# Optimization experiments

Hardware: AMD Instinct MI355X
Metric: run time of the kernel (lower is better)

The kernel has to match this reference:

```python
import jax, jax.numpy as jnp
from jax import lax
import numpy as np

N_ATOMS, N_BONDS, N_GRAPHS = 8192, 32768, 256
EMBED, HIDDEN, DEPTH = 32, 256, 10
ATOM_VOCAB, BOND_VOCAB = 200, 10


def setup_inputs() -> dict:
    key = jax.random.key(0)
    ks = jax.random.split(key, 16)
    f = lambda k, *sh: jax.random.normal(k, sh, dtype=jnp.float32) * 0.05
    return {
        "atom_features": jax.random.randint(ks[0], (N_ATOMS,), 0, ATOM_VOCAB),
        "bond_features": jax.random.randint(ks[1], (N_BONDS,), 0, BOND_VOCAB),
        "adjacency_matrix": jax.random.randint(ks[2], (N_ATOMS, N_ATOMS), 0, 2, dtype=jnp.int32),
        "batch_indices": jax.random.randint(ks[3], (N_ATOMS,), 0, N_GRAPHS),
        "atom_emb": f(ks[4], ATOM_VOCAB, EMBED),
        "bond_emb": f(ks[5], BOND_VOCAB, EMBED),
        "msg_W": f(ks[6], DEPTH, HIDDEN, 2 * EMBED),
        "msg_b": f(ks[7], DEPTH, HIDDEN),
        "gru_Wih": f(ks[8], DEPTH, 3 * EMBED, HIDDEN),
        "gru_Whh": f(ks[9], DEPTH, 3 * EMBED, EMBED),
        "gru_bih": f(ks[10], DEPTH, 3 * EMBED),
        "gru_bhh": f(ks[11], DEPTH, 3 * EMBED),
        "pool_W": f(ks[12], HIDDEN, EMBED),
        "pool_b": f(ks[13], HIDDEN),
    }


def _gmpn(atom_emb, bond_emb, msg_W, msg_b, gru_Wih, gru_Whh, gru_bih, gru_bhh,
          pool_W, pool_b, atom_features, bond_features, adjacency_matrix, batch_indices):
    H = atom_emb[atom_features]                       # [N, E]
    A = (adjacency_matrix > 0).astype(H.dtype)        # [N, N] 0/1
    deg = A.sum(axis=1)                               # [N]
    has_nb = deg > 0
    inv_deg = jnp.where(has_nb, 1.0 / jnp.maximum(deg, 1.0), 0.0)[:, None]

    def layer(h, params):
        W, b, wih, whh, b_ih, b_hh = params
        # mean_j Linear([h_i ; h_j]) = W1 h_i + W2 mean_j h_j + b
        neigh_mean = (A @ h) * inv_deg                # [N, E]
        W1, W2 = W[:, :EMBED], W[:, EMBED:]
        msg = h @ W1.T + neigh_mean @ W2.T + b        # [N, HIDDEN]
        msg = jnp.where(has_nb[:, None], msg, 0.0)    # zero message if no neighbors
        # single-step GRU: input=msg, hidden state=h
        gi = msg @ wih.T + b_ih
        gh = h @ whh.T + b_hh
        ir, iz, inn = jnp.split(gi, 3, axis=-1)
        hr, hz, hn = jnp.split(gh, 3, axis=-1)
        r = jax.nn.sigmoid(ir + hr)
        z = jax.nn.sigmoid(iz + hz)
        n = jnp.tanh(inn + r * hn)
        h_new = (1.0 - z) * n + z * h                 # [N, E]
        return h_new, None

    H, _ = lax.scan(layer, H, (msg_W, msg_b, gru_Wih, gru_Whh, gru_bih, gru_bhh))

    # per-graph mean pooling (zeros for empty graphs), then global_pool linear
    seg_sum = jax.ops.segment_sum(H, batch_indices, num_segments=N_GRAPHS)
    cnt = jax.ops.segment_sum(jnp.ones((H.shape[0],), H.dtype), batch_indices, num_segments=N_GRAPHS)
    graph_mean = jnp.where(cnt[:, None] > 0, seg_sum / jnp.maximum(cnt, 1.0)[:, None], 0.0)
    graph_embeddings = graph_mean @ pool_W.T + pool_b  # [G, HIDDEN]

    bond_embeddings = bond_emb[bond_features]          # [B, E]
    return H, bond_embeddings, graph_embeddings


def reference(atom_features, bond_features, adjacency_matrix, batch_indices,
              atom_emb, bond_emb, msg_W, msg_b, gru_Wih, gru_Whh, gru_bih, gru_bhh,
              pool_W, pool_b):
    return _gmpn(atom_emb, bond_emb, msg_W, msg_b, gru_Wih, gru_Whh, gru_bih, gru_bhh,
                 pool_W, pool_b, atom_features, bond_features, adjacency_matrix, batch_indices)
```

## Files before the change

kernel.cpp:

```cpp
#include <hip/hip_runtime.h>
#include <stdint.h>

typedef __bf16 bf16x8 __attribute__((ext_vector_type(8)));
typedef float f32x4 __attribute__((ext_vector_type(4)));

__device__ __forceinline__ float b2f(unsigned short u){
  unsigned int t = ((unsigned int)u) << 16;
  return __builtin_bit_cast(float, t);
}
__device__ __forceinline__ unsigned short f2b(float f){
  unsigned int x = __builtin_bit_cast(unsigned int, f);
  x = x + 0x7FFFu + ((x >> 16) & 1u);
  return (unsigned short)(x >> 16);
}
__device__ __forceinline__ void spread8(unsigned int B, unsigned int w[4]){
  unsigned int m = __umul24(B, 0x8001u);
  w[0] = __umul24(m & 0x00010001u, 0x3F80u);
  w[1] = __umul24(m & 0x00040004u, 0x0FE0u);
  w[2] = __umul24(m & 0x00100010u, 0x03F8u);
  w[3] = __umul24(m & 0x00400040u, 0x00FEu);
}
__device__ __forceinline__ float fsig(float x){ return 1.f/(1.f + __expf(-x)); }
__device__ __forceinline__ float ftanh(float x){ return 1.f - 2.f/(__expf(2.f*x) + 1.f); }

__global__ void k_prep(const void* s_msgW, const void* s_msgb, const void* s_wih,
                       const void* s_whh, const void* s_bih, const void* s_bhh,
                       const void* s_poolW, const void* s_poolb,
                       const unsigned short* __restrict__ aemb_u16,
                       unsigned short* __restrict__ cw,
                       int* __restrict__ deg, float* __restrict__ seg,
                       float* __restrict__ cnt, int* __restrict__ flag){
  int b = blockIdx.x, t = threadIdx.x;
  unsigned int uu = aemb_u16[2*t];
  int e = (int)((uu >> 7) & 0xFF);
  unsigned long long vote = __ballot(e >= 100 && e <= 127);
  int isb = (__popcll(vote) > 32) ? 1 : 0;
  if (b < 1771){
    int id = b*256 + t;
    if (id < 453248){
      const void* src; int off;
      if      (id < 163840){ src = s_msgW;  off = id; }
      else if (id < 166400){ src = s_msgb;  off = id - 163840; }
      else if (id < 412160){ src = s_wih;   off = id - 166400; }
      else if (id < 442880){ src = s_whh;   off = id - 412160; }
      else if (id < 443840){ src = s_bih;   off = id - 442880; }
      else if (id < 444800){ src = s_bhh;   off = id - 443840; }
      else if (id < 452992){ src = s_poolW; off = id - 444800; }
      else                 { src = s_poolb; off = id - 452992; }
      cw[id] = isb ? ((const unsigned short*)src)[off]
                   : f2b(((const float*)src)[off]);
    }
  } else {
    int id2 = (b - 1771)*256 + t;
    if (id2 < 8192){ deg[id2] = 0; seg[id2] = 0.f; }
    if (id2 < 256) cnt[id2] = 0.f;
    if (b == 1771 && t == 0) flag[0] = isb;
  }
}

__global__ void k_pack(const int* __restrict__ adj, unsigned int* __restrict__ mask3,
                       int* __restrict__ deg){
  int tid = blockIdx.x*256 + threadIdx.x;
  int rb  = tid >> 12;
  int rem = tid & 4095;
  int kgg = rem >> 6;
  int L   = rem & 63;
  int lc = L & 15, q = L >> 4;
  int row = rb*16 + lc;
  const int* arow = adj + (size_t)row*8192 + kgg*128 + q*8;
  unsigned int dw = 0; int pc = 0;
  #pragma unroll
  for (int s=0;s<4;s++){
    const int* p = arow + s*32;
    unsigned int b = 0;
    #pragma unroll
    for (int t=0;t<8;t++) b |= (p[t] > 0 ? 1u : 0u) << t;
    dw |= b << (8*s);
    pc += __popc(b);
  }
  mask3[tid] = dw;
  pc += __shfl_xor(pc, 16);
  pc += __shfl_xor(pc, 32);
  if (q == 0) atomicAdd(deg + row, pc);
}

__global__ void k_bond(const int* __restrict__ bft, const void* __restrict__ braw,
                       const int* __restrict__ flag,
                       unsigned short* __restrict__ outB16, float* __restrict__ outB32){
  int id = blockIdx.x*256 + threadIdx.x;
  int e = id >> 5, c = id & 31;
  int idx = bft[e]*32 + c;
  if (flag[0]) outB16[id] = ((const unsigned short*)braw)[idx];
  else         outB32[id] = ((const float*)braw)[idx];
}

__global__ void k_embed(const int* __restrict__ af, const void* __restrict__ araw,
                        const int* __restrict__ flag,
                        float* __restrict__ hf32, uint4* __restrict__ hfrag){
  __shared__ __align__(16) float sh[512];
  int t = threadIdx.x;
  int r = t >> 5, c = t & 31;
  int row = blockIdx.x*16 + r;
  int idx = af[row]*32 + c;
  float f;
  if (flag[0]) f = b2f(((const unsigned short*)araw)[idx]);
  else         f = ((const float*)araw)[idx];
  hf32[row*32 + c] = f;
  sh[r*32 + c] = f;
  __syncthreads();
  if (t < 64){
    int nt = t >> 5, Lq = t & 31;
    int ks32 = blockIdx.x >> 1, half = blockIdx.x & 1;
    int col = nt*16 + (Lq & 15);
    int rbase = (Lq >> 4)*8;
    unsigned int w[4];
    #pragma unroll
    for (int p=0;p<4;p++){
      unsigned int lo = f2b(sh[(rbase + 2*p    )*32 + col]);
      unsigned int hi = f2b(sh[(rbase + 2*p + 1)*32 + col]);
      w[p] = lo | (hi << 16);
    }
    hfrag[(ks32*2 + nt)*64 + half*32 + Lq] = make_uint4(w[0],w[1],w[2],w[3]);
  }
}

__launch_bounds__(512)
__global__ void k_layer(const unsigned int* __restrict__ mask3,
                        const uint4* __restrict__ hfragIn,
                        unsigned int* __restrict__ hfragOut,
                        float* __restrict__ hf32,
                        const int* __restrict__ deg,
                        const unsigned short* __restrict__ msgW,
                        const unsigned short* __restrict__ msgb,
                        const unsigned short* __restrict__ wih,
                        const unsigned short* __restrict__ whh,
                        const unsigned short* __restrict__ bih,
                        const unsigned short* __restrict__ bhh,
                        const int* __restrict__ bidx,
                        float* __restrict__ seg, float* __restrict__ cnt,
                        unsigned short* __restrict__ out16, float* __restrict__ out32,
                        const int* __restrict__ flag, int last)
{
  __shared__ __align__(16) char uni[33792];
  __shared__ __align__(16) unsigned short sA[32][72];
  __shared__ __align__(16) unsigned short smsg[32][264];
  __shared__ int sdeg[32];

  const int t = threadIdx.x;
  const int b = blockIdx.x;
  const int w = t >> 6, L = t & 63;
  const int q = L >> 4, lc = L & 15;
  const int rowbase = b*32;

  const int r0 = t >> 4;
  const int cl = t & 15;
  const int r  = rowbase + r0;
  const int isb = flag[0];
  const int dgr = deg[r];
  const float invr = dgr > 0 ? 1.f/(float)dgr : 0.f;
  float h0 = hf32[r*32 + cl];
  float h1 = hf32[r*32 + 16 + cl];
  sA[r0][cl]    = f2b(h0);
  sA[r0][16+cl] = f2b(h1);
  if (cl == 0) sdeg[r0] = dgr;

  {
    f32x4 a00={0,0,0,0}, a01={0,0,0,0}, a10={0,0,0,0}, a11={0,0,0,0};
    const unsigned int* mp = mask3 + (size_t)b*8192 + w*512 + L;
    const uint4* bp = hfragIn + (size_t)w*4096 + L;
    for (int g=0; g<8; g++){
      unsigned int mw0 = mp[g*64];
      unsigned int mw1 = mp[4096 + g*64];
      #pragma unroll
      for (int s=0; s<4; s++){
        int ks = g*4 + s;
        uint4 u0 = bp[ks*128];
        uint4 u1 = bp[ks*128 + 64];
        union { unsigned int u[4]; bf16x8 v; } A0, A1, B0, B1;
        spread8((mw0 >> (8*s)) & 0xFFu, A0.u);
        spread8((mw1 >> (8*s)) & 0xFFu, A1.u);
        B0.u[0]=u0.x; B0.u[1]=u0.y; B0.u[2]=u0.z; B0.u[3]=u0.w;
        B1.u[0]=u1.x; B1.u[1]=u1.y; B1.u[2]=u1.z; B1.u[3]=u1.w;
        a00 = __builtin_amdgcn_mfma_f32_16x16x32_bf16(A0.v, B0.v, a00, 0,0,0);
        a01 = __builtin_amdgcn_mfma_f32_16x16x32_bf16(A0.v, B1.v, a01, 0,0,0);
        a10 = __builtin_amdgcn_mfma_f32_16x16x32_bf16(A1.v, B0.v, a10, 0,0,0);
        a11 = __builtin_amdgcn_mfma_f32_16x16x32_bf16(A1.v, B1.v, a11, 0,0,0);
      }
    }
    float* sp = (float*)uni + w*1056;
    #pragma unroll
    for (int rg=0; rg<4; rg++){
      int rw = q*4 + rg;
      sp[rw*33 + lc]         = a00[rg];
      sp[rw*33 + 16 + lc]    = a01[rg];
      sp[(16+rw)*33 + lc]    = a10[rg];
      sp[(16+rw)*33 + 16+lc] = a11[rg];
    }
  }
  __syncthreads();
  {
    const float* spf = (const float*)uni;
    float s0 = 0.f, s1 = 0.f;
    #pragma unroll
    for (int ww=0; ww<8; ww++){
      s0 += spf[ww*1056 + r0*33 + cl];
      s1 += spf[ww*1056 + r0*33 + 16 + cl];
    }
    sA[r0][32+cl] = f2b(s0*invr);
    sA[r0][48+cl] = f2b(s1*invr);
  }
  __syncthreads();
  {
    int rt = w & 1, ntb = (w >> 1)*4;
    union { uint4 u; bf16x8 v; } A0, A1;
    A0.u = *(const uint4*)&sA[rt*16 + lc][q*8];
    A1.u = *(const uint4*)&sA[rt*16 + lc][32 + q*8];
    #pragma unroll
    for (int i=0; i<4; i++){
      int nt = ntb + i;
      union { uint4 u; bf16x8 v; } B0, B1;
      B0.u = *(const uint4*)(msgW + (size_t)(nt*16 + lc)*64 + q*8);
      B1.u = *(const uint4*)(msgW + (size_t)(nt*16 + lc)*64 + 32 + q*8);
      f32x4 am = {0,0,0,0};
      am = __builtin_amdgcn_mfma_f32_16x16x32_bf16(A0.v, B0.v, am, 0,0,0);
      am = __builtin_amdgcn_mfma_f32_16x16x32_bf16(A1.v, B1.v, am, 0,0,0);
      float bv = b2f(msgb[nt*16 + lc]);
      #pragma unroll
      for (int rg=0; rg<4; rg++){
        int rw = rt*16 + q*4 + rg;
        float v = am[rg] + bv;
        if (sdeg[rw] == 0) v = 0.f;
        smsg[rw][nt*16 + lc] = f2b(v);
      }
    }
  }
  __syncthreads();
  {
    float* sgi = (float*)uni;
    float* sgh = (float*)(uni + 12800);
    if (w < 6){
      int nt = w;
      f32x4 g0 = {0,0,0,0}, g1 = {0,0,0,0};
      #pragma unroll
      for (int ks=0; ks<8; ks++){
        union { uint4 u; bf16x8 v; } A0, A1, B;
        B.u  = *(const uint4*)(wih + (size_t)(nt*16 + lc)*256 + ks*32 + q*8);
        A0.u = *(const uint4*)&smsg[lc][ks*32 + q*8];
        A1.u = *(const uint4*)&smsg[16 + lc][ks*32 + q*8];
        g0 = __builtin_amdgcn_mfma_f32_16x16x32_bf16(A0.v, B.v, g0, 0,0,0);
        g1 = __builtin_amdgcn_mfma_f32_16x16x32_bf16(A1.v, B.v, g1, 0,0,0);
      }
      #pragma unroll
      for (int rg=0; rg<4; rg++){
        sgi[(q*4+rg)*100      + nt*16 + lc] = g0[rg];
        sgi[(16+q*4+rg)*100   + nt*16 + lc] = g1[rg];
      }
    } else {
      int rt = w - 6;
      union { uint4 u; bf16x8 v; } A;
      A.u = *(const uint4*)&sA[rt*16 + lc][q*8];
      #pragma unroll
      for (int nt=0; nt<6; nt++){
        union { uint4 u; bf16x8 v; } B;
        B.u = *(const uint4*)(whh + (size_t)(nt*16 + lc)*32 + q*8);
        f32x4 hh = {0,0,0,0};
        hh = __builtin_amdgcn_mfma_f32_16x16x32_bf16(A.v, B.v, hh, 0,0,0);
        #pragma unroll
        for (int rg=0; rg<4; rg++)
          sgh[(rt*16 + q*4+rg)*100 + nt*16 + lc] = hh[rg];
      }
    }
  }
  __syncthreads();
  {
    const float* sgi = (const float*)uni;
    const float* sgh = (const float*)(uni + 12800);
    float ir0 = sgi[r0*100 + cl]    + b2f(bih[cl]),    hr0 = sgh[r0*100 + cl]    + b2f(bhh[cl]);
    float iz0 = sgi[r0*100 + 32+cl] + b2f(bih[32+cl]), hz0 = sgh[r0*100 + 32+cl] + b2f(bhh[32+cl]);
    float in0 = sgi[r0*100 + 64+cl] + b2f(bih[64+cl]), hn0 = sgh[r0*100 + 64+cl] + b2f(bhh[64+cl]);
    float ir1 = sgi[r0*100 + 16+cl] + b2f(bih[16+cl]), hr1 = sgh[r0*100 + 16+cl] + b2f(bhh[16+cl]);
    float iz1 = sgi[r0*100 + 48+cl] + b2f(bih[48+cl]), hz1 = sgh[r0*100 + 48+cl] + b2f(bhh[48+cl]);
    float in1 = sgi[r0*100 + 80+cl] + b2f(bih[80+cl]), hn1 = sgh[r0*100 + 80+cl] + b2f(bhh[80+cl]);
    float rr0 = fsig(ir0 + hr0), zz0 = fsig(iz0 + hz0);
    float rr1 = fsig(ir1 + hr1), zz1 = fsig(iz1 + hz1);
    float nn0 = ftanh(in0 + rr0*hn0);
    float nn1 = ftanh(in1 + rr1*hn1);
    h0 = (1.f - zz0)*nn0 + zz0*h0;
    h1 = (1.f - zz1)*nn1 + zz1*h1;
    hf32[r*32 + cl]      = h0;
    hf32[r*32 + 16 + cl] = h1;
    unsigned int m0 = f2b(h0), m1 = f2b(h1);
    unsigned int p0 = (unsigned int)__shfl_xor((int)m0, 16);
    unsigned int p1 = (unsigned int)__shfl_xor((int)m1, 16);
    if ((r & 1) == 0){
      int ks32 = r >> 5;
      int Lf = ((r >> 3) & 3)*16 + cl;
      int pidx = (r & 7) >> 1;
      hfragOut[((ks32*2 + 0)*64 + Lf)*4 + pidx] = m0 | (p0 << 16);
      hfragOut[((ks32*2 + 1)*64 + Lf)*4 + pidx] = m1 | (p1 << 16);
    }
    if (last){
      if (isb){ out16[r*32 + cl] = (unsigned short)m0; out16[r*32 + 16 + cl] = (unsigned short)m1; }
      else    { out32[r*32 + cl] = h0; out32[r*32 + 16 + cl] = h1; }
      int gb = bidx[r];
      atomicAdd(seg + gb*32 + cl, h0);
      atomicAdd(seg + gb*32 + 16 + cl, h1);
      if (cl == 0) atomicAdd(cnt + gb, 1.f);
    }
  }
}

__global__ void k_pool(const float* __restrict__ seg, const float* __restrict__ cnt,
                       const unsigned short* __restrict__ pw, const unsigned short* __restrict__ pb,
                       const int* __restrict__ flag,
                       unsigned short* __restrict__ outG16, float* __restrict__ outG32){
  int g = blockIdx.x, o = threadIdx.x;
  float cv = cnt[g];
  float ic = cv > 0.f ? 1.f/cv : 0.f;
  float s = 0.f;
  #pragma unroll
  for (int c=0;c<32;c++) s += seg[g*32+c]*ic*b2f(pw[o*32+c]);
  s += b2f(pb[o]);
  if (flag[0]) outG16[g*256 + o] = f2b(s);
  else         outG32[g*256 + o] = s;
}

extern "C" void kernel_launch(void* const* d_in, const int* in_sizes, int n_in,
                              void* d_out, int out_size, void* d_ws, size_t ws_size,
                              hipStream_t stream){
  const int* af   = (const int*)d_in[0];
  const int* bft  = (const int*)d_in[1];
  const int* adj  = (const int*)d_in[2];
  const int* bidx = (const int*)d_in[3];

  char* ws = (char*)d_ws;
  unsigned int*   mask3  = (unsigned int*)(ws + 0);
  unsigned int*   hfrag0 = (unsigned int*)(ws + 8388608);
  unsigned int*   hfrag1 = (unsigned int*)(ws + 8912896);
  float*          hf32   = (float*)(ws + 9437184);
  int*            deg    = (int*)(ws + 10485760);
  float*          seg    = (float*)(ws + 10518528);
  float*          cnt    = (float*)(ws + 10551296);
  int*            flag   = (int*)(ws + 10552320);
  unsigned short* cw     = (unsigned short*)(ws + 10552384);

  unsigned short* o16 = (unsigned short*)d_out;
  float*          o32 = (float*)d_out;

  k_prep<<<1803, 256, 0, stream>>>(d_in[6], d_in[7], d_in[8], d_in[9], d_in[10],
                                   d_in[11], d_in[12], d_in[13],
                                   (const unsigned short*)d_in[4],
                                   cw, deg, seg, cnt, flag);
  k_pack<<<8192, 256, 0, stream>>>(adj, mask3, deg);
  k_bond<<<4096, 256, 0, stream>>>(bft, d_in[5], flag, o16 + 262144, o32 + 262144);
  k_embed<<<512, 512, 0, stream>>>(af, d_in[4], flag, hf32, (uint4*)hfrag0);

  for (int d = 0; d < 10; d++){
    const uint4*  hin  = (const uint4*)((d & 1) ? hfrag1 : hfrag0);
    unsigned int* hout = (d & 1) ? hfrag0 : hfrag1;
    k_layer<<<256, 512, 0, stream>>>(mask3, hin, hout, hf32, deg,
                                     cw + (size_t)d*16384,        cw + 163840 + d*256,
                                     cw + 166400 + (size_t)d*24576, cw + 412160 + d*3072,
                                     cw + 442880 + d*96,          cw + 443840 + d*96,
                                     bidx, seg, cnt, o16, o32, flag, (d == 9) ? 1 : 0);
  }
  k_pool<<<256, 256, 0, stream>>>(seg, cnt, cw + 444800, cw + 452992, flag,
                                  o16 + 1310720, o32 + 1310720);
}
```

Baseline: 535.3 us.

## Halve rows per layer block to double grid, vectorize adjacency packing loads

The layer kernel now handles 16 atom rows per block instead of 32 and launches 512 blocks, so more CUs are busy on a 256-CU-class GPU. Each block's shared memory roughly halves and a min-blocks launch bound is added to raise occupancy. The trade-off is that every block now streams the full hfrag B operand for half as many rows, doubling total B-operand reads from L2. The adjacency pack kernel also switches to int4 vector loads.

```diff
diff --git a/kernel.cpp b/kernel.cpp
--- a/kernel.cpp
+++ b/kernel.cpp
@@ -67,14 +67,20 @@
   int L   = rem & 63;
   int lc = L & 15, q = L >> 4;
   int row = rb*16 + lc;
-  const int* arow = adj + (size_t)row*8192 + kgg*128 + q*8;
+  const int4* p4 = (const int4*)(adj + (size_t)row*8192 + kgg*128 + q*8);
   unsigned int dw = 0; int pc = 0;
   #pragma unroll
   for (int s=0;s<4;s++){
-    const int* p = arow + s*32;
-    unsigned int b = 0;
-    #pragma unroll
-    for (int t=0;t<8;t++) b |= (p[t] > 0 ? 1u : 0u) << t;
+    int4 u = p4[s*8];
+    int4 v = p4[s*8 + 1];
+    unsigned int b = (unsigned int)(u.x > 0)
+                   | ((unsigned int)(u.y > 0) << 1)
+                   | ((unsigned int)(u.z > 0) << 2)
+                   | ((unsigned int)(u.w > 0) << 3)
+                   | ((unsigned int)(v.x > 0) << 4)
+                   | ((unsigned int)(v.y > 0) << 5)
+                   | ((unsigned int)(v.z > 0) << 6)
+                   | ((unsigned int)(v.w > 0) << 7);
     dw |= b << (8*s);
     pc += __popc(b);
   }
@@ -124,7 +130,7 @@
   }
 }
 
-__launch_bounds__(512)
+__launch_bounds__(512, 4)
 __global__ void k_layer(const unsigned int* __restrict__ mask3,
                         const uint4* __restrict__ hfragIn,
                         unsigned int* __restrict__ hfragOut,
@@ -141,83 +147,71 @@
                         unsigned short* __restrict__ out16, float* __restrict__ out32,
                         const int* __restrict__ flag, int last)
 {
-  __shared__ __align__(16) char uni[33792];
-  __shared__ __align__(16) unsigned short sA[32][72];
-  __shared__ __align__(16) unsigned short smsg[32][264];
-  __shared__ int sdeg[32];
+  __shared__ __align__(16) char uni[16896];
+  __shared__ __align__(16) unsigned short sA[16][72];
+  __shared__ __align__(16) unsigned short smsg[16][264];
+  __shared__ int sdeg[16];
 
   const int t = threadIdx.x;
   const int b = blockIdx.x;
   const int w = t >> 6, L = t & 63;
   const int q = L >> 4, lc = L & 15;
-  const int rowbase = b*32;
-
-  const int r0 = t >> 4;
-  const int cl = t & 15;
+  const int rowbase = b*16;
+
+  const int r0 = t >> 5;
+  const int c  = t & 31;
   const int r  = rowbase + r0;
   const int isb = flag[0];
   const int dgr = deg[r];
   const float invr = dgr > 0 ? 1.f/(float)dgr : 0.f;
-  float h0 = hf32[r*32 + cl];
-  float h1 = hf32[r*32 + 16 + cl];
-  sA[r0][cl]    = f2b(h0);
-  sA[r0][16+cl] = f2b(h1);
-  if (cl == 0) sdeg[r0] = dgr;
-
-  {
-    f32x4 a00={0,0,0,0}, a01={0,0,0,0}, a10={0,0,0,0}, a11={0,0,0,0};
-    const unsigned int* mp = mask3 + (size_t)b*8192 + w*512 + L;
+  float h = hf32[r*32 + c];
+  sA[r0][c] = f2b(h);
+  if (c == 0) sdeg[r0] = dgr;
+
+  {
+    f32x4 a00={0,0,0,0}, a01={0,0,0,0};
+    const unsigned int* mp = mask3 + (size_t)b*4096 + w*512 + L;
     const uint4* bp = hfragIn + (size_t)w*4096 + L;
     for (int g=0; g<8; g++){
       unsigned int mw0 = mp[g*64];
-      unsigned int mw1 = mp[4096 + g*64];
       #pragma unroll
       for (int s=0; s<4; s++){
         int ks = g*4 + s;
         uint4 u0 = bp[ks*128];
         uint4 u1 = bp[ks*128 + 64];
-        union { unsigned int u[4]; bf16x8 v; } A0, A1, B0, B1;
+        union { unsigned int u[4]; bf16x8 v; } A0, B0, B1;
         spread8((mw0 >> (8*s)) & 0xFFu, A0.u);
-        spread8((mw1 >> (8*s)) & 0xFFu, A1.u);
         B0.u[0]=u0.x; B0.u[1]=u0.y; B0.u[2]=u0.z; B0.u[3]=u0.w;
         B1.u[0]=u1.x; B1.u[1]=u1.y; B1.u[2]=u1.z; B1.u[3]=u1.w;
         a00 = __builtin_amdgcn_mfma_f32_16x16x32_bf16(A0.v, B0.v, a00, 0,0,0);
         a01 = __builtin_amdgcn_mfma_f32_16x16x32_bf16(A0.v, B1.v, a01, 0,0,0);
-        a10 = __builtin_amdgcn_mfma_f32_16x16x32_bf16(A1.v, B0.v, a10, 0,0,0);
-        a11 = __builtin_amdgcn_mfma_f32_16x16x32_bf16(A1.v, B1.v, a11, 0,0,0);
       }
     }
-    float* sp = (float*)uni + w*1056;
+    float* sp = (float*)uni + w*528;
     #pragma unroll
     for (int rg=0; rg<4; rg++){
       int rw = q*4 + rg;
-      sp[rw*33 + lc]         = a00[rg];
-      sp[rw*33 + 16 + lc]    = a01[rg];
-      sp[(16+rw)*33 + lc]    = a10[rg];
-      sp[(16+rw)*33 + 16+lc] = a11[rg];
+      sp[rw*33 + lc]      = a00[rg];
+      sp[rw*33 + 16 + lc] = a01[rg];
     }
   }
   __syncthreads();
   {
     const float* spf = (const float*)uni;
-    float s0 = 0.f, s1 = 0.f;
+    float s = 0.f;
     #pragma unroll
-    for (int ww=0; ww<8; ww++){
-      s0 += spf[ww*1056 + r0*33 + cl];
-      s1 += spf[ww*1056 + r0*33 + 16 + cl];
-    }
-    sA[r0][32+cl] = f2b(s0*invr);
-    sA[r0][48+cl] = f2b(s1*invr);
-  }
-  __syncthreads();
-  {
-    int rt = w & 1, ntb = (w >> 1)*4;
+    for (int ww=0; ww<8; ww++)
+      s += spf[ww*528 + r0*33 + c];
+    sA[r0][32+c] = f2b(s*invr);
+  }
+  __syncthreads();
+  {
     union { uint4 u; bf16x8 v; } A0, A1;
-    A0.u = *(const uint4*)&sA[rt*16 + lc][q*8];
-    A1.u = *(const uint4*)&sA[rt*16 + lc][32 + q*8];
+    A0.u = *(const uint4*)&sA[lc][q*8];
+    A1.u = *(const uint4*)&sA[lc][32 + q*8];
     #pragma unroll
-    for (int i=0; i<4; i++){
-      int nt = ntb + i;
+    for (int i=0; i<2; i++){
+      int nt = w*2 + i;
       union { uint4 u; bf16x8 v; } B0, B1;
       B0.u = *(const uint4*)(msgW + (size_t)(nt*16 + lc)*64 + q*8);
       B1.u = *(const uint4*)(msgW + (size_t)(nt*16 + lc)*64 + 32 + q*8);
@@ -227,7 +221,7 @@
       float bv = b2f(msgb[nt*16 + lc]);
       #pragma unroll
       for (int rg=0; rg<4; rg++){
-        int rw = rt*16 + q*4 + rg;
+        int rw = q*4 + rg;
         float v = am[rg] + bv;
         if (sdeg[rw] == 0) v = 0.f;
         smsg[rw][nt*16 + lc] = f2b(v);
@@ -237,75 +231,62 @@
   __syncthreads();
   {
     float* sgi = (float*)uni;
-    float* sgh = (float*)(uni + 12800);
+    float* sgh = (float*)(uni + 6400);
     if (w < 6){
       int nt = w;
-      f32x4 g0 = {0,0,0,0}, g1 = {0,0,0,0};
+      f32x4 g0 = {0,0,0,0};
       #pragma unroll
       for (int ks=0; ks<8; ks++){
-        union { uint4 u; bf16x8 v; } A0, A1, B;
+        union { uint4 u; bf16x8 v; } A0, B;
         B.u  = *(const uint4*)(wih + (size_t)(nt*16 + lc)*256 + ks*32 + q*8);
         A0.u = *(const uint4*)&smsg[lc][ks*32 + q*8];
-        A1.u = *(const uint4*)&smsg[16 + lc][ks*32 + q*8];
         g0 = __builtin_amdgcn_mfma_f32_16x16x32_bf16(A0.v, B.v, g0, 0,0,0);
-        g1 = __builtin_amdgcn_mfma_f32_16x16x32_bf16(A1.v, B.v, g1, 0,0,0);
       }
       #pragma unroll
-      for (int rg=0; rg<4; rg++){
-        sgi[(q*4+rg)*100      + nt*16 + lc] = g0[rg];
-        sgi[(16+q*4+rg)*100   + nt*16 + lc] = g1[rg];
-      }
+      for (int rg=0; rg<4; rg++)
+        sgi[(q*4+rg)*100 + nt*16 + lc] = g0[rg];
     } else {
-      int rt = w - 6;
       union { uint4 u; bf16x8 v; } A;
-      A.u = *(const uint4*)&sA[rt*16 + lc][q*8];
-      #pragma unroll
-      for (int nt=0; nt<6; nt++){
+      A.u = *(const uint4*)&sA[lc][q*8];
+      #pragma unroll
+      for (int i=0; i<3; i++){
+        int nt = (w - 6)*3 + i;
         union { uint4 u; bf16x8 v; } B;
         B.u = *(const uint4*)(whh + (size_t)(nt*16 + lc)*32 + q*8);
         f32x4 hh = {0,0,0,0};
         hh = __builtin_amdgcn_mfma_f32_16x16x32_bf16(A.v, B.v, hh, 0,0,0);
         #pragma unroll
         for (int rg=0; rg<4; rg++)
-          sgh[(rt*16 + q*4+rg)*100 + nt*16 + lc] = hh[rg];
+          sgh[(q*4+rg)*100 + nt*16 + lc] = hh[rg];
       }
     }
   }
   __syncthreads();
   {
     const float* sgi = (const float*)uni;
-    const float* sgh = (const float*)(uni + 12800);
-    float ir0 = sgi[r0*100 + cl]    + b2f(bih[cl]),    hr0 = sgh[r0*100 + cl]    + b2f(bhh[cl]);
-    float iz0 = sgi[r0*100 + 32+cl] + b2f(bih[32+cl]), hz0 = sgh[r0*100 + 32+cl] + b2f(bhh[32+cl]);
-    float in0 = sgi[r0*100 + 64+cl] + b2f(bih[64+cl]), hn0 = sgh[r0*100 + 64+cl] + b2f(bhh[64+cl]);
-    float ir1 = sgi[r0*100 + 16+cl] + b2f(bih[16+cl]), hr1 = sgh[r0*100 + 16+cl] + b2f(bhh[16+cl]);
-    float iz1 = sgi[r0*100 + 48+cl] + b2f(bih[48+cl]), hz1 = sgh[r0*100 + 48+cl] + b2f(bhh[48+cl]);
-    float in1 = sgi[r0*100 + 80+cl] + b2f(bih[80+cl]), hn1 = sgh[r0*100 + 80+cl] + b2f(bhh[80+cl]);
-    float rr0 = fsig(ir0 + hr0), zz0 = fsig(iz0 + hz0);
-    float rr1 = fsig(ir1 + hr1), zz1 = fsig(iz1 + hz1);
-    float nn0 = ftanh(in0 + rr0*hn0);
-    float nn1 = ftanh(in1 + rr1*hn1);
-    h0 = (1.f - zz0)*nn0 + zz0*h0;
-    h1 = (1.f - zz1)*nn1 + zz1*h1;
-    hf32[r*32 + cl]      = h0;
-    hf32[r*32 + 16 + cl] = h1;
-    unsigned int m0 = f2b(h0), m1 = f2b(h1);
-    unsigned int p0 = (unsigned int)__shfl_xor((int)m0, 16);
-    unsigned int p1 = (unsigned int)__shfl_xor((int)m1, 16);
+    const float* sgh = (const float*)(uni + 6400);
+    float ir = sgi[r0*100 +      c] + b2f(bih[     c]), hr = sgh[r0*100 +      c] + b2f(bhh[     c]);
+    float iz = sgi[r0*100 + 32 + c] + b2f(bih[32 + c]), hz = sgh[r0*100 + 32 + c] + b2f(bhh[32 + c]);
+    float in = sgi[r0*100 + 64 + c] + b2f(bih[64 + c]), hn = sgh[r0*100 + 64 + c] + b2f(bhh[64 + c]);
+    float rr = fsig(ir + hr), zz = fsig(iz + hz);
+    float nn = ftanh(in + rr*hn);
+    h = (1.f - zz)*nn + zz*h;
+    hf32[r*32 + c] = h;
+    unsigned int m = f2b(h);
+    unsigned int p = (unsigned int)__shfl_xor((int)m, 32);
     if ((r & 1) == 0){
       int ks32 = r >> 5;
-      int Lf = ((r >> 3) & 3)*16 + cl;
+      int nt = c >> 4, cl2 = c & 15;
+      int Lf = ((r >> 3) & 3)*16 + cl2;
       int pidx = (r & 7) >> 1;
-      hfragOut[((ks32*2 + 0)*64 + Lf)*4 + pidx] = m0 | (p0 << 16);
-      hfragOut[((ks32*2 + 1)*64 + Lf)*4 + pidx] = m1 | (p1 << 16);
+      hfragOut[((ks32*2 + nt)*64 + Lf)*4 + pidx] = m | (p << 16);
     }
     if (last){
-      if (isb){ out16[r*32 + cl] = (unsigned short)m0; out16[r*32 + 16 + cl] = (unsigned short)m1; }
-      else    { out32[r*32 + cl] = h0; out32[r*32 + 16 + cl] = h1; }
+      if (isb) out16[r*32 + c] = (unsigned short)m;
+      else     out32[r*32 + c] = h;
       int gb = bidx[r];
-      atomicAdd(seg + gb*32 + cl, h0);
-      atomicAdd(seg + gb*32 + 16 + cl, h1);
-      if (cl == 0) atomicAdd(cnt + gb, 1.f);
+      atomicAdd(seg + gb*32 + c, h);
+      if (c == 0) atomicAdd(cnt + gb, 1.f);
     }
   }
 }
@@ -358,7 +339,7 @@
   for (int d = 0; d < 10; d++){
     const uint4*  hin  = (const uint4*)((d & 1) ? hfrag1 : hfrag0);
     unsigned int* hout = (d & 1) ? hfrag0 : hfrag1;
-    k_layer<<<256, 512, 0, stream>>>(mask3, hin, hout, hf32, deg,
+    k_layer<<<512, 512, 0, stream>>>(mask3, hin, hout, hf32, deg,
                                      cw + (size_t)d*16384,        cw + 163840 + d*256,
                                      cw + 166400 + (size_t)d*24576, cw + 412160 + d*3072,
                                      cw + 442880 + d*96,          cw + 443840 + d*96,
```

Result: slower. 573.2 us (+7.1%).

## Fuse ten layer launches into one persistent cooperative kernel with grid sync

Applied to the files above, without the earlier changes.

Replaces the ten per-layer kernel launches with a single cooperative kernel that loops over depth and uses a grid-wide barrier between layers. The hidden state h now stays in registers across layers instead of being written to and reread from global fp32 memory each layer. This removes launch gaps and redundant global traffic. In exchange it adds grid-sync overhead and requires all 256 blocks of 512 threads to be co-resident, which cooperative launch must satisfy.

```diff
diff --git a/kernel.cpp b/kernel.cpp
--- a/kernel.cpp
+++ b/kernel.cpp
@@ -1,5 +1,8 @@
 #include <hip/hip_runtime.h>
+#include <hip/hip_cooperative_groups.h>
 #include <stdint.h>
+
+namespace cg = cooperative_groups;
 
 typedef __bf16 bf16x8 __attribute__((ext_vector_type(8)));
 typedef float f32x4 __attribute__((ext_vector_type(4)));
@@ -125,22 +128,19 @@
 }
 
 __launch_bounds__(512)
-__global__ void k_layer(const unsigned int* __restrict__ mask3,
-                        const uint4* __restrict__ hfragIn,
-                        unsigned int* __restrict__ hfragOut,
-                        float* __restrict__ hf32,
-                        const int* __restrict__ deg,
-                        const unsigned short* __restrict__ msgW,
-                        const unsigned short* __restrict__ msgb,
-                        const unsigned short* __restrict__ wih,
-                        const unsigned short* __restrict__ whh,
-                        const unsigned short* __restrict__ bih,
-                        const unsigned short* __restrict__ bhh,
-                        const int* __restrict__ bidx,
-                        float* __restrict__ seg, float* __restrict__ cnt,
-                        unsigned short* __restrict__ out16, float* __restrict__ out32,
-                        const int* __restrict__ flag, int last)
+__global__ void k_layers(const unsigned int* __restrict__ mask3,
+                         unsigned int* __restrict__ hfrag0,
+                         unsigned int* __restrict__ hfrag1,
+                         const float* __restrict__ hf32,
+                         const int* __restrict__ deg,
+                         const unsigned short* __restrict__ cw,
+                         const int* __restrict__ bidx,
+                         float* __restrict__ seg, float* __restrict__ cnt,
+                         unsigned short* __restrict__ out16, float* __restrict__ out32,
+                         const int* __restrict__ flag)
 {
+  cg::grid_group gg = cg::this_grid();
+
   __shared__ __align__(16) char uni[33792];
   __shared__ __align__(16) unsigned short sA[32][72];
   __shared__ __align__(16) unsigned short smsg[32][264];
@@ -160,153 +160,165 @@
   const float invr = dgr > 0 ? 1.f/(float)dgr : 0.f;
   float h0 = hf32[r*32 + cl];
   float h1 = hf32[r*32 + 16 + cl];
-  sA[r0][cl]    = f2b(h0);
-  sA[r0][16+cl] = f2b(h1);
   if (cl == 0) sdeg[r0] = dgr;
 
-  {
-    f32x4 a00={0,0,0,0}, a01={0,0,0,0}, a10={0,0,0,0}, a11={0,0,0,0};
-    const unsigned int* mp = mask3 + (size_t)b*8192 + w*512 + L;
-    const uint4* bp = hfragIn + (size_t)w*4096 + L;
-    for (int g=0; g<8; g++){
-      unsigned int mw0 = mp[g*64];
-      unsigned int mw1 = mp[4096 + g*64];
-      #pragma unroll
-      for (int s=0; s<4; s++){
-        int ks = g*4 + s;
-        uint4 u0 = bp[ks*128];
-        uint4 u1 = bp[ks*128 + 64];
-        union { unsigned int u[4]; bf16x8 v; } A0, A1, B0, B1;
-        spread8((mw0 >> (8*s)) & 0xFFu, A0.u);
-        spread8((mw1 >> (8*s)) & 0xFFu, A1.u);
-        B0.u[0]=u0.x; B0.u[1]=u0.y; B0.u[2]=u0.z; B0.u[3]=u0.w;
-        B1.u[0]=u1.x; B1.u[1]=u1.y; B1.u[2]=u1.z; B1.u[3]=u1.w;
-        a00 = __builtin_amdgcn_mfma_f32_16x16x32_bf16(A0.v, B0.v, a00, 0,0,0);
-        a01 = __builtin_amdgcn_mfma_f32_16x16x32_bf16(A0.v, B1.v, a01, 0,0,0);
-        a10 = __builtin_amdgcn_mfma_f32_16x16x32_bf16(A1.v, B0.v, a10, 0,0,0);
-        a11 = __builtin_amdgcn_mfma_f32_16x16x32_bf16(A1.v, B1.v, a11, 0,0,0);
-      }
-    }
-    float* sp = (float*)uni + w*1056;
-    #pragma unroll
-    for (int rg=0; rg<4; rg++){
-      int rw = q*4 + rg;
-      sp[rw*33 + lc]         = a00[rg];
-      sp[rw*33 + 16 + lc]    = a01[rg];
-      sp[(16+rw)*33 + lc]    = a10[rg];
-      sp[(16+rw)*33 + 16+lc] = a11[rg];
-    }
-  }
-  __syncthreads();
-  {
-    const float* spf = (const float*)uni;
-    float s0 = 0.f, s1 = 0.f;
-    #pragma unroll
-    for (int ww=0; ww<8; ww++){
-      s0 += spf[ww*1056 + r0*33 + cl];
-      s1 += spf[ww*1056 + r0*33 + 16 + cl];
-    }
-    sA[r0][32+cl] = f2b(s0*invr);
-    sA[r0][48+cl] = f2b(s1*invr);
-  }
-  __syncthreads();
-  {
-    int rt = w & 1, ntb = (w >> 1)*4;
-    union { uint4 u; bf16x8 v; } A0, A1;
-    A0.u = *(const uint4*)&sA[rt*16 + lc][q*8];
-    A1.u = *(const uint4*)&sA[rt*16 + lc][32 + q*8];
-    #pragma unroll
-    for (int i=0; i<4; i++){
-      int nt = ntb + i;
-      union { uint4 u; bf16x8 v; } B0, B1;
-      B0.u = *(const uint4*)(msgW + (size_t)(nt*16 + lc)*64 + q*8);
-      B1.u = *(const uint4*)(msgW + (size_t)(nt*16 + lc)*64 + 32 + q*8);
-      f32x4 am = {0,0,0,0};
-      am = __builtin_amdgcn_mfma_f32_16x16x32_bf16(A0.v, B0.v, am, 0,0,0);
-      am = __builtin_amdgcn_mfma_f32_16x16x32_bf16(A1.v, B1.v, am, 0,0,0);
-      float bv = b2f(msgb[nt*16 + lc]);
+  for (int d = 0; d < 10; ++d){
+    const unsigned short* msgW = cw + (size_t)d*16384;
+    const unsigned short* msgb = cw + 163840 + d*256;
+    const unsigned short* wih  = cw + 166400 + (size_t)d*24576;
+    const unsigned short* whh  = cw + 412160 + d*3072;
+    const unsigned short* bih  = cw + 442880 + d*96;
+    const unsigned short* bhh  = cw + 443840 + d*96;
+    const uint4*  hfragIn  = (const uint4*)((d & 1) ? hfrag1 : hfrag0);
+    unsigned int* hfragOut = (d & 1) ? hfrag0 : hfrag1;
+    const int last = (d == 9);
+
+    sA[r0][cl]    = f2b(h0);
+    sA[r0][16+cl] = f2b(h1);
+
+    {
+      f32x4 a00={0,0,0,0}, a01={0,0,0,0}, a10={0,0,0,0}, a11={0,0,0,0};
+      const unsigned int* mp = mask3 + (size_t)b*8192 + w*512 + L;
+      const uint4* bp = hfragIn + (size_t)w*4096 + L;
+      for (int g=0; g<8; g++){
+        unsigned int mw0 = mp[g*64];
+        unsigned int mw1 = mp[4096 + g*64];
+        #pragma unroll
+        for (int s=0; s<4; s++){
+          int ks = g*4 + s;
+          uint4 u0 = bp[ks*128];
+          uint4 u1 = bp[ks*128 + 64];
+          union { unsigned int u[4]; bf16x8 v; } A0, A1, B0, B1;
+          spread8((mw0 >> (8*s)) & 0xFFu, A0.u);
+          spread8((mw1 >> (8*s)) & 0xFFu, A1.u);
+          B0.u[0]=u0.x; B0.u[1]=u0.y; B0.u[2]=u0.z; B0.u[3]=u0.w;
+          B1.u[0]=u1.x; B1.u[1]=u1.y; B1.u[2]=u1.z; B1.u[3]=u1.w;
+          a00 = __builtin_amdgcn_mfma_f32_16x16x32_bf16(A0.v, B0.v, a00, 0,0,0);
+          a01 = __builtin_amdgcn_mfma_f32_16x16x32_bf16(A0.v, B1.v, a01, 0,0,0);
+          a10 = __builtin_amdgcn_mfma_f32_16x16x32_bf16(A1.v, B0.v, a10, 0,0,0);
+          a11 = __builtin_amdgcn_mfma_f32_16x16x32_bf16(A1.v, B1.v, a11, 0,0,0);
+        }
+      }
+      float* sp = (float*)uni + w*1056;
       #pragma unroll
       for (int rg=0; rg<4; rg++){
-        int rw = rt*16 + q*4 + rg;
-        float v = am[rg] + bv;
-        if (sdeg[rw] == 0) v = 0.f;
-        smsg[rw][nt*16 + lc] = f2b(v);
-      }
-    }
-  }
-  __syncthreads();
-  {
-    float* sgi = (float*)uni;
-    float* sgh = (float*)(uni + 12800);
-    if (w < 6){
-      int nt = w;
-      f32x4 g0 = {0,0,0,0}, g1 = {0,0,0,0};
+        int rw = q*4 + rg;
+        sp[rw*33 + lc]         = a00[rg];
+        sp[rw*33 + 16 + lc]    = a01[rg];
+        sp[(16+rw)*33 + lc]    = a10[rg];
+        sp[(16+rw)*33 + 16+lc] = a11[rg];
+      }
+    }
+    __syncthreads();
+    {
+      const float* spf = (const float*)uni;
+      float s0 = 0.f, s1 = 0.f;
       #pragma unroll
-      for (int ks=0; ks<8; ks++){
-        union { uint4 u; bf16x8 v; } A0, A1, B;
-        B.u  = *(const uint4*)(wih + (size_t)(nt*16 + lc)*256 + ks*32 + q*8);
-        A0.u = *(const uint4*)&smsg[lc][ks*32 + q*8];
-        A1.u = *(const uint4*)&smsg[16 + lc][ks*32 + q*8];
-        g0 = __builtin_amdgcn_mfma_f32_16x16x32_bf16(A0.v, B.v, g0, 0,0,0);
-        g1 = __builtin_amdgcn_mfma_f32_16x16x32_bf16(A1.v, B.v, g1, 0,0,0);
-      }
+      for (int ww=0; ww<8; ww++){
+        s0 += spf[ww*1056 + r0*33 + cl];
+        s1 += spf[ww*1056 + r0*33 + 16 + cl];
+      }
+      sA[r0][32+cl] = f2b(s0*invr);
+      sA[r0][48+cl] = f2b(s1*invr);
+    }
+    __syncthreads();
+    {
+      int rt = w & 1, ntb = (w >> 1)*4;
+      union { uint4 u; bf16x8 v; } A0, A1;
+      A0.u = *(const uint4*)&sA[rt*16 + lc][q*8];
+      A1.u = *(const uint4*)&sA[rt*16 + lc][32 + q*8];
       #pragma unroll
-      for (int rg=0; rg<4; rg++){
-        sgi[(q*4+rg)*100      + nt*16 + lc] = g0[rg];
-        sgi[(16+q*4+rg)*100   + nt*16 + lc] = g1[rg];
-      }
-    } else {
-      int rt = w - 6;
-      union { uint4 u; bf16x8 v; } A;
-      A.u = *(const uint4*)&sA[rt*16 + lc][q*8];
-      #pragma unroll
-      for (int nt=0; nt<6; nt++){
-        union { uint4 u; bf16x8 v; } B;
-        B.u = *(const uint4*)(whh + (size_t)(nt*16 + lc)*32 + q*8);
-        f32x4 hh = {0,0,0,0};
-        hh = __builtin_amdgcn_mfma_f32_16x16x32_bf16(A.v, B.v, hh, 0,0,0);
-        #pragma unroll
-        for (int rg=0; rg<4; rg++)
-          sgh[(rt*16 + q*4+rg)*100 + nt*16 + lc] = hh[rg];
-      }
-    }
-  }
-  __syncthreads();
-  {
-    const float* sgi = (const float*)uni;
-    const float* sgh = (const float*)(uni + 12800);
-    float ir0 = sgi[r0*100 + cl]    + b2f(bih[cl]),    hr0 = sgh[r0*100 + cl]    + b2f(bhh[cl]);
-    float iz0 = sgi[r0*100 + 32+cl] + b2f(bih[32+cl]), hz0 = sgh[r0*100 + 32+cl] + b2f(bhh[32+cl]);
-    float in0 = sgi[r0*100 + 64+cl] + b2f(bih[64+cl]), hn0 = sgh[r0*100 + 64+cl] + b2f(bhh[64+cl]);
-    float ir1 = sgi[r0*100 + 16+cl] + b2f(bih[16+cl]), hr1 = sgh[r0*100 + 16+cl] + b2f(bhh[16+cl]);
-    float iz1 = sgi[r0*100 + 48+cl] + b2f(bih[48+cl]), hz1 = sgh[r0*100 + 48+cl] + b2f(bhh[48+cl]);
-    float in1 = sgi[r0*100 + 80+cl] + b2f(bih[80+cl]), hn1 = sgh[r0*100 + 80+cl] + b2f(bhh[80+cl]);
-    float rr0 = fsig(ir0 + hr0), zz0 = fsig(iz0 + hz0);
-    float rr1 = fsig(ir1 + hr1), zz1 = fsig(iz1 + hz1);
-    float nn0 = ftanh(in0 + rr0*hn0);
-    float nn1 = ftanh(in1 + rr1*hn1);
-    h0 = (1.f - zz0)*nn0 + zz0*h0;
-    h1 = (1.f - zz1)*nn1 + zz1*h1;
-    hf32[r*32 + cl]      = h0;
-    hf32[r*32 + 16 + cl] = h1;
-    unsigned int m0 = f2b(h0), m1 = f2b(h1);
-    unsigned int p0 = (unsigned int)__shfl_xor((int)m0, 16);
-    unsigned int p1 = (unsigned int)__shfl_xor((int)m1, 16);
-    if ((r & 1) == 0){
-      int ks32 = r >> 5;
-      int Lf = ((r >> 3) & 3)*16 + cl;
-      int pidx = (r & 7) >> 1;
-      hfragOut[((ks32*2 + 0)*64 + Lf)*4 + pidx] = m0 | (p0 << 16);
-      hfragOut[((ks32*2 + 1)*64 + Lf)*4 + pidx] = m1 | (p1 << 16);
-    }
-    if (last){
-      if (isb){ out16[r*32 + cl] = (unsigned short)m0; out16[r*32 + 16 + cl] = (unsigned short)m1; }
-      else    { out32[r*32 + cl] = h0; out32[r*32 + 16 + cl] = h1; }
-      int gb = bidx[r];
-      atomicAdd(seg + gb*32 + cl, h0);
-      atomicAdd(seg + gb*32 + 16 + cl, h1);
-      if (cl == 0) atomicAdd(cnt + gb, 1.f);
-    }
+      for (int i=0; i<4; i++){
+        int nt = ntb + i;
+        union { uint4 u; bf16x8 v; } B0, B1;
+        B0.u = *(const uint4*)(msgW + (size_t)(nt*16 + lc)*64 + q*8);
+        B1.u = *(const uint4*)(msgW + (size_t)(nt*16 + lc)*64 + 32 + q*8);
+        f32x4 am = {0,0,0,0};
+        am = __builtin_amdgcn_mfma_f32_16x16x32_bf16(A0.v, B0.v, am, 0,0,0);
+        am = __builtin_amdgcn_mfma_f32_16x16x32_bf16(A1.v, B1.v, am, 0,0,0);
+        float bv = b2f(msgb[nt*16 + lc]);
+        #pragma unroll
+        for (int rg=0; rg<4; rg++){
+          int rw = rt*16 + q*4 + rg;
+          float v = am[rg] + bv;
+          if (sdeg[rw] == 0) v = 0.f;
+          smsg[rw][nt*16 + lc] = f2b(v);
+        }
+      }
+    }
+    __syncthreads();
+    {
+      float* sgi = (float*)uni;
+      float* sgh = (float*)(uni + 12800);
+      if (w < 6){
+        int nt = w;
+        f32x4 g0 = {0,0,0,0}, g1 = {0,0,0,0};
+        #pragma unroll
+        for (int ks=0; ks<8; ks++){
+          union { uint4 u; bf16x8 v; } A0, A1, B;
+          B.u  = *(const uint4*)(wih + (size_t)(nt*16 + lc)*256 + ks*32 + q*8);
+          A0.u = *(const uint4*)&smsg[lc][ks*32 + q*8];
+          A1.u = *(const uint4*)&smsg[16 + lc][ks*32 + q*8];
+          g0 = __builtin_amdgcn_mfma_f32_16x16x32_bf16(A0.v, B.v, g0, 0,0,0);
+          g1 = __builtin_amdgcn_mfma_f32_16x16x32_bf16(A1.v, B.v, g1, 0,0,0);
+        }
+        #pragma unroll
+        for (int rg=0; rg<4; rg++){
+          sgi[(q*4+rg)*100      + nt*16 + lc] = g0[rg];
+          sgi[(16+q*4+rg)*100   + nt*16 + lc] = g1[rg];
+        }
+      } else {
+        int rt = w - 6;
+        union { uint4 u; bf16x8 v; } A;
+        A.u = *(const uint4*)&sA[rt*16 + lc][q*8];
+        #pragma unroll
+        for (int nt=0; nt<6; nt++){
+          union { uint4 u; bf16x8 v; } B;
+          B.u = *(const uint4*)(whh + (size_t)(nt*16 + lc)*32 + q*8);
+          f32x4 hh = {0,0,0,0};
+          hh = __builtin_amdgcn_mfma_f32_16x16x32_bf16(A.v, B.v, hh, 0,0,0);
+          #pragma unroll
+          for (int rg=0; rg<4; rg++)
+            sgh[(rt*16 + q*4+rg)*100 + nt*16 + lc] = hh[rg];
+        }
+      }
+    }
+    __syncthreads();
+    {
+      const float* sgi = (const float*)uni;
+      const float* sgh = (const float*)(uni + 12800);
+      float ir0 = sgi[r0*100 + cl]    + b2f(bih[cl]),    hr0 = sgh[r0*100 + cl]    + b2f(bhh[cl]);
+      float iz0 = sgi[r0*100 + 32+cl] + b2f(bih[32+cl]), hz0 = sgh[r0*100 + 32+cl] + b2f(bhh[32+cl]);
+      float in0 = sgi[r0*100 + 64+cl] + b2f(bih[64+cl]), hn0 = sgh[r0*100 + 64+cl] + b2f(bhh[64+cl]);
+      float ir1 = sgi[r0*100 + 16+cl] + b2f(bih[16+cl]), hr1 = sgh[r0*100 + 16+cl] + b2f(bhh[16+cl]);
+      float iz1 = sgi[r0*100 + 48+cl] + b2f(bih[48+cl]), hz1 = sgh[r0*100 + 48+cl] + b2f(bhh[48+cl]);
+      float in1 = sgi[r0*100 + 80+cl] + b2f(bih[80+cl]), hn1 = sgh[r0*100 + 80+cl] + b2f(bhh[80+cl]);
+      float rr0 = fsig(ir0 + hr0), zz0 = fsig(iz0 + hz0);
+      float rr1 = fsig(ir1 + hr1), zz1 = fsig(iz1 + hz1);
+      float nn0 = ftanh(in0 + rr0*hn0);
+      float nn1 = ftanh(in1 + rr1*hn1);
+      h0 = (1.f - zz0)*nn0 + zz0*h0;
+      h1 = (1.f - zz1)*nn1 + zz1*h1;
+      unsigned int m0 = f2b(h0), m1 = f2b(h1);
+      unsigned int p0 = (unsigned int)__shfl_xor((int)m0, 16);
+      unsigned int p1 = (unsigned int)__shfl_xor((int)m1, 16);
+      if ((r & 1) == 0){
+        int ks32 = r >> 5;
+        int Lf = ((r >> 3) & 3)*16 + cl;
+        int pidx = (r & 7) >> 1;
+        hfragOut[((ks32*2 + 0)*64 + Lf)*4 + pidx] = m0 | (p0 << 16);
+        hfragOut[((ks32*2 + 1)*64 + Lf)*4 + pidx] = m1 | (p1 << 16);
+      }
+      if (last){
+        if (isb){ out16[r*32 + cl] = (unsigned short)m0; out16[r*32 + 16 + cl] = (unsigned short)m1; }
+        else    { out32[r*32 + cl] = h0; out32[r*32 + 16 + cl] = h1; }
+        int gb = bidx[r];
+        atomicAdd(seg + gb*32 + cl, h0);
+        atomicAdd(seg + gb*32 + 16 + cl, h1);
+        if (cl == 0) atomicAdd(cnt + gb, 1.f);
+      }
+    }
+    if (d < 9) gg.sync();
   }
 }
 
@@ -355,15 +367,12 @@
   k_bond<<<4096, 256, 0, stream>>>(bft, d_in[5], flag, o16 + 262144, o32 + 262144);
   k_embed<<<512, 512, 0, stream>>>(af, d_in[4], flag, hf32, (uint4*)hfrag0);
 
-  for (int d = 0; d < 10; d++){
-    const uint4*  hin  = (const uint4*)((d & 1) ? hfrag1 : hfrag0);
-    unsigned int* hout = (d & 1) ? hfrag0 : hfrag1;
-    k_layer<<<256, 512, 0, stream>>>(mask3, hin, hout, hf32, deg,
-                                     cw + (size_t)d*16384,        cw + 163840 + d*256,
-                                     cw + 166400 + (size_t)d*24576, cw + 412160 + d*3072,
-                                     cw + 442880 + d*96,          cw + 443840 + d*96,
-                                     bidx, seg, cnt, o16, o32, flag, (d == 9) ? 1 : 0);
-  }
+  void* kargs[] = { (void*)&mask3, (void*)&hfrag0, (void*)&hfrag1, (void*)&hf32,
+                    (void*)&deg, (void*)&cw, (void*)&bidx, (void*)&seg, (void*)&cnt,
+                    (void*)&o16, (void*)&o32, (void*)&flag };
+  hipLaunchCooperativeKernel(reinterpret_cast<void*>(k_layers),
+                             dim3(256), dim3(512), kargs, 0, stream);
+
   k_pool<<<256, 256, 0, stream>>>(seg, cnt, cw + 444800, cw + 452992, flag,
                                   o16 + 1310720, o32 + 1310720);
 }
```

Result: slower. 835.1 us (+56.0%).
